# Optimization experiments

Measured on AMD Instinct MI355X. Metric: run time of the kernel, lower is better.

## Reference

```python
import jax, jax.numpy as jnp
import numpy as np

N_NODES = 100000
N_EDGES = 1600000
N_GRAPHS = 1024


def gcn_conv(x, W, b, src, dst, n_nodes):
    """PyG-style GCNConv: add self-loops, symmetric deg^-1/2 normalization,
    linear transform, scatter-add aggregation, bias."""
    h = x @ W  # [N, out]
    ones = jnp.ones(src.shape[0], dtype=h.dtype)
    deg = jax.ops.segment_sum(ones, dst, num_segments=n_nodes) + 1.0  # +1 self-loop
    dinv = jax.lax.rsqrt(deg)  # deg^-1/2, deg >= 1 so safe
    norm = dinv[src] * dinv[dst]  # [E]
    msg = h[src] * norm[:, None]  # gather + scale
    agg = jax.ops.segment_sum(msg, dst, num_segments=n_nodes)  # scatter-add
    # self-loop contribution: norm_ii = dinv_i^2
    return agg + h * (dinv * dinv)[:, None] + b


def setup_inputs() -> dict:
    key = jax.random.key(0)
    ks = jax.random.split(key, 12)
    x = jax.random.normal(ks[0], (N_NODES, 5), dtype=jnp.float32)
    src = jax.random.randint(ks[1], (N_EDGES,), 0, N_NODES)
    dst = jax.random.randint(ks[2], (N_EDGES,), 0, N_NODES)
    batch = jnp.sort(jax.random.randint(ks[3], (N_NODES,), 0, N_GRAPHS))
    def glorot(k, shp):
        lim = float(np.sqrt(6.0 / (shp[0] + shp[1])))
        return jax.random.uniform(k, shp, jnp.float32, -lim, lim)
    return {
        "x": x, "src": src, "dst": dst, "batch": batch,
        "W1": glorot(ks[4], (5, 16)),  "b1": jnp.zeros((16,), jnp.float32),
        "W2": glorot(ks[5], (16, 32)), "b2": jnp.zeros((32,), jnp.float32),
        "W3": glorot(ks[6], (32, 64)), "b3": jnp.zeros((64,), jnp.float32),
        "Wfc": glorot(ks[7], (64, 2)), "bfc": jnp.zeros((2,), jnp.float32),
    }


def reference(x, src, dst, batch, W1, b1, W2, b2, W3, b3, Wfc, bfc):
    h = jax.nn.relu(gcn_conv(x, W1, b1, src, dst, N_NODES))
    h = jax.nn.relu(gcn_conv(h, W2, b2, src, dst, N_NODES))
    h = jax.nn.relu(gcn_conv(h, W3, b3, src, dst, N_NODES))
    # global mean pool over graphs
    summed = jax.ops.segment_sum(h, batch, num_segments=N_GRAPHS)  # [G, 64]
    counts = jax.ops.segment_sum(jnp.ones(h.shape[0], h.dtype), batch, num_segments=N_GRAPHS)
    pooled = summed / jnp.maximum(counts, 1.0)[:, None]
    logits = pooled @ Wfc + bfc  # [G, 2]
    return jax.nn.log_softmax(logits, axis=1)
```

## Files before the change

### kernel.cpp

```cpp
#include <hip/hip_runtime.h>


#define BLK 256
#define CH 4096
#define EPT (CH / BLK)
#define NB 256
#define GSH 9
#define GSZ 512


__device__ inline float bfu_lo(unsigned int w) { return __uint_as_float(w << 16); }
__device__ inline float bfu_hi(unsigned int w) { return __uint_as_float(w & 0xffff0000u); }
__device__ inline unsigned int f2bf(float f) {
    unsigned int w = __float_as_uint(f);
    return (w + 0x7fffu + ((w >> 16) & 1u)) >> 16;
}
__device__ inline unsigned int pack2(float a, float b) {
    return f2bf(a) | (f2bf(b) << 16);
}


__global__ void hist1_kernel(const int* __restrict__ dst, int* __restrict__ cnt,
                             int E, int nChunks) {
    __shared__ int h[NB];
    int t = threadIdx.x, b = blockIdx.x;
    h[t] = 0;
    __syncthreads();
    int base = b * CH;
#pragma unroll
    for (int j = 0; j < EPT; ++j) {
        int e = base + j * BLK + t;
        if (e < E) atomicAdd(&h[dst[e] >> GSH], 1);
    }
    __syncthreads();
    cnt[(size_t)t * nChunks + b] = h[t];
}

__global__ void seg_scan_kernel(int* __restrict__ cnt, int* __restrict__ bucketTot,
                                int nChunks) {
    __shared__ int part[256];
    int b = blockIdx.x, t = threadIdx.x;
    size_t base = (size_t)b * nChunks;
    int per = (nChunks + 255) / 256;
    int lo = t * per, hi = lo + per < nChunks ? lo + per : nChunks;
    int sum = 0;
    for (int i = lo; i < hi; ++i) sum += cnt[base + i];
    part[t] = sum;
    __syncthreads();
    for (int off = 1; off < 256; off <<= 1) {
        int x = (t >= off) ? part[t - off] : 0;
        __syncthreads();
        if (t >= off) part[t] += x;
        __syncthreads();
    }
    int run = part[t] - sum;
    for (int i = lo; i < hi; ++i) { int v = cnt[base + i]; cnt[base + i] = run; run += v; }
    if (t == 255) bucketTot[b] = part[255];
}

__global__ void bucket_scan_kernel(const int* __restrict__ bucketTot,
                                   int* __restrict__ groupBeg, int E) {
    __shared__ int part[256];
    int t = threadIdx.x;
    int v = bucketTot[t];
    part[t] = v;
    __syncthreads();
    for (int off = 1; off < 256; off <<= 1) {
        int x = (t >= off) ? part[t - off] : 0;
        __syncthreads();
        if (t >= off) part[t] += x;
        __syncthreads();
    }
    groupBeg[t] = part[t] - v;
    if (t == 0) groupBeg[NB] = E;
}

__global__ void scatter1_kernel(const int* __restrict__ src, const int* __restrict__ dst,
                                const int* __restrict__ cnt, const int* __restrict__ groupBeg,
                                int* __restrict__ pe, int E, int nChunks) {
    __shared__ int offs[NB];
    int t = threadIdx.x, b = blockIdx.x;
    offs[t] = cnt[(size_t)t * nChunks + b] + groupBeg[t];
    __syncthreads();
    int base = b * CH;
#pragma unroll
    for (int j = 0; j < EPT; ++j) {
        int e = base + j * BLK + t;
        if (e < E) {
            int d = dst[e];
            int p = atomicAdd(&offs[d >> GSH], 1);
            pe[p] = ((d & (GSZ - 1)) << 17) | src[e];
        }
    }
}


__global__ void group_csr_kernel(const int* __restrict__ pe, const int* __restrict__ groupBeg,
                                 int* __restrict__ col, int* __restrict__ row_ptr,
                                 float* __restrict__ dinv, const float* __restrict__ x,
                                 uint4* __restrict__ xa, int N, int E) {
    __shared__ int hist[GSZ];
    __shared__ int scn[GSZ];
    __shared__ int part[256];
    int g = blockIdx.x, t = threadIdx.x;
    hist[t] = 0; hist[t + 256] = 0;
    __syncthreads();
    int lo = groupBeg[g], hi = groupBeg[g + 1];
    for (int e = lo + t; e < hi; e += BLK)
        atomicAdd(&hist[pe[e] >> 17], 1);
    __syncthreads();
    int a0 = hist[2 * t], a1 = hist[2 * t + 1];
    int s2 = a0 + a1;
    part[t] = s2;
    __syncthreads();
    for (int off = 1; off < 256; off <<= 1) {
        int xx = (t >= off) ? part[t - off] : 0;
        __syncthreads();
        if (t >= off) part[t] += xx;
        __syncthreads();
    }
    int excl = part[t] - s2;
    scn[2 * t] = excl;
    scn[2 * t + 1] = excl + a0;
    __syncthreads();
#pragma unroll
    for (int i = t; i < GSZ; i += BLK) {
        int d = (g << GSH) + i;
        if (d < N) {
            row_ptr[d] = lo + scn[i];
            float di = rsqrtf((float)hist[i] + 1.0f);
            dinv[d] = di;
            const float* r = x + (size_t)d * 5;
            uint4 u;
            u.x = pack2(r[0] * di, r[1] * di);
            u.y = pack2(r[2] * di, r[3] * di);
            u.z = pack2(r[4] * di, 0.f);
            u.w = 0u;
            xa[d] = u;
        }
    }
    if (g == 0 && t == 0) row_ptr[N] = E;
    __syncthreads();
    hist[t] = scn[t]; hist[t + 256] = scn[t + 256];
    __syncthreads();
    for (int e = lo + t; e < hi; e += BLK) {
        int v = pe[e];
        int p = atomicAdd(&hist[v >> 17], 1);
        col[lo + p] = v & 0x1FFFF;
    }
}


template <int F, int FIN, int FOUT, int CAP, bool PRESCALE_OUT>
__global__ void fused_layer_kernel(const int* __restrict__ row_ptr, const int* __restrict__ col,
                                   const uint4* __restrict__ xb, const float* __restrict__ W,
                                   const float* __restrict__ bias, const float* __restrict__ dinv,
                                   uint2* __restrict__ outb, int N) {
    constexpr int TPN = F / 8;
    constexpr int NPB = 256 / TPN;
    constexpr int RQ  = F / 8;
    constexpr int QO  = FOUT / 4;
    constexpr int STR = F + 1;
    __shared__ int lcol[CAP];
    __shared__ int lrp[NPB + 1];
    __shared__ __align__(16) float gl[NPB * STR];
    __shared__ __align__(16) float wl[FIN * FOUT];
    __shared__ __align__(16) float bl[FOUT];
    int t = threadIdx.x;
    int n0 = blockIdx.x * NPB;
    for (int i = t; i <= NPB; i += 256) lrp[i] = row_ptr[min(n0 + i, N)];
    for (int i = t; i < FIN * FOUT / 4; i += 256)
        ((float4*)wl)[i] = ((const float4*)W)[i];
    for (int i = t; i < FOUT; i += 256) bl[i] = bias[i];
    __syncthreads();
    int base = lrp[0];
    int total = lrp[NPB] - base;
    int stage = total < CAP ? total : CAP;
    for (int i = t; i < stage; i += 256) lcol[i] = col[base + i];
    __syncthreads();
    {
        int ln = t / TPN, q = t % TPN;
        int n = n0 + ln;
        if (n < N) {
            float acc[8];
            uint4 u = xb[(size_t)n * RQ + q];
            acc[0] = bfu_lo(u.x); acc[1] = bfu_hi(u.x);
            acc[2] = bfu_lo(u.y); acc[3] = bfu_hi(u.y);
            acc[4] = bfu_lo(u.z); acc[5] = bfu_hi(u.z);
            acc[6] = bfu_lo(u.w); acc[7] = bfu_hi(u.w);
            int beg = lrp[ln] - base, end = lrp[ln + 1] - base;
            int stop = end < stage ? end : stage;
            int e = beg;
            for (; e + 3 < stop; e += 4) {
                int s0 = lcol[e], s1 = lcol[e + 1], s2 = lcol[e + 2], s3 = lcol[e + 3];
                uint4 u0 = xb[(size_t)s0 * RQ + q];
                uint4 u1 = xb[(size_t)s1 * RQ + q];
                uint4 u2 = xb[(size_t)s2 * RQ + q];
                uint4 u3 = xb[(size_t)s3 * RQ + q];
                acc[0] += bfu_lo(u0.x) + bfu_lo(u1.x) + bfu_lo(u2.x) + bfu_lo(u3.x);
                acc[1] += bfu_hi(u0.x) + bfu_hi(u1.x) + bfu_hi(u2.x) + bfu_hi(u3.x);
                acc[2] += bfu_lo(u0.y) + bfu_lo(u1.y) + bfu_lo(u2.y) + bfu_lo(u3.y);
                acc[3] += bfu_hi(u0.y) + bfu_hi(u1.y) + bfu_hi(u2.y) + bfu_hi(u3.y);
                acc[4] += bfu_lo(u0.z) + bfu_lo(u1.z) + bfu_lo(u2.z) + bfu_lo(u3.z);
                acc[5] += bfu_hi(u0.z) + bfu_hi(u1.z) + bfu_hi(u2.z) + bfu_hi(u3.z);
                acc[6] += bfu_lo(u0.w) + bfu_lo(u1.w) + bfu_lo(u2.w) + bfu_lo(u3.w);
                acc[7] += bfu_hi(u0.w) + bfu_hi(u1.w) + bfu_hi(u2.w) + bfu_hi(u3.w);
            }
            for (; e < end; ++e) {
                int s = (e < stage) ? lcol[e] : col[base + e];
                uint4 uu = xb[(size_t)s * RQ + q];
                acc[0] += bfu_lo(uu.x); acc[1] += bfu_hi(uu.x);
                acc[2] += bfu_lo(uu.y); acc[3] += bfu_hi(uu.y);
                acc[4] += bfu_lo(uu.z); acc[5] += bfu_hi(uu.z);
                acc[6] += bfu_lo(uu.w); acc[7] += bfu_hi(uu.w);
            }
            float* gr = gl + ln * STR + q * 8;
#pragma unroll
            for (int j = 0; j < 8; ++j) gr[j] = acc[j];
        }
    }
    __syncthreads();
    for (int task = t; task < NPB * QO; task += 256) {
        int ln2 = task / QO, qq = task % QO;
        int n2 = n0 + ln2;
        if (n2 >= N) continue;
        float di = dinv[n2];
        const float* row = gl + ln2 * STR;
        float4 acc = make_float4(0.f, 0.f, 0.f, 0.f);
#pragma unroll
        for (int k = 0; k < FIN; ++k) {
            float rk = row[k];
            float4 wk = *(const float4*)(wl + k * FOUT + 4 * qq);
            acc.x = fmaf(rk, wk.x, acc.x);
            acc.y = fmaf(rk, wk.y, acc.y);
            acc.z = fmaf(rk, wk.z, acc.z);
            acc.w = fmaf(rk, wk.w, acc.w);
        }
        float4 bq = *(const float4*)(bl + 4 * qq);
        float4 v;
        v.x = fmaxf(di * acc.x + bq.x, 0.f);
        v.y = fmaxf(di * acc.y + bq.y, 0.f);
        v.z = fmaxf(di * acc.z + bq.z, 0.f);
        v.w = fmaxf(di * acc.w + bq.w, 0.f);
        if (PRESCALE_OUT) { v.x *= di; v.y *= di; v.z *= di; v.w *= di; }
        uint2 o;
        o.x = pack2(v.x, v.y);
        o.y = pack2(v.z, v.w);
        outb[(size_t)n2 * QO + qq] = o;
    }
}


__global__ void bounds_kernel(const int* __restrict__ batch, int* __restrict__ start,
                              int N, int G) {
    int g = blockIdx.x * blockDim.x + threadIdx.x;
    if (g > G) return;
    if (g == G) { start[G] = N; return; }
    int lo = 0, hi = N;
    while (lo < hi) {
        int mid = (lo + hi) >> 1;
        if (batch[mid] < g) lo = mid + 1; else hi = mid;
    }
    start[g] = lo;
}

__global__ void pool_head_kernel(const unsigned int* __restrict__ h, const int* __restrict__ start,
                                 const float* __restrict__ Wfc, const float* __restrict__ bfc,
                                 float* __restrict__ out) {
    __shared__ float part[8][64];
    int g = blockIdx.x;
    int t = threadIdx.x;
    int u = t & 31, w = t >> 5;
    int s = start[g], e = start[g + 1];
    float a0 = 0.f, a1 = 0.f;
    for (int n = s + w; n < e; n += 8) {
        unsigned int word = h[(size_t)n * 32 + u];
        a0 += bfu_lo(word);
        a1 += bfu_hi(word);
    }
    part[w][2 * u]     = a0;
    part[w][2 * u + 1] = a1;
    __syncthreads();
    if (t < 64) {
        float p = 0.f;
#pragma unroll
        for (int w2 = 0; w2 < 8; ++w2) p += part[w2][t];
        p /= fmaxf((float)(e - s), 1.0f);
        float l0 = p * Wfc[t * 2 + 0];
        float l1 = p * Wfc[t * 2 + 1];
#pragma unroll
        for (int off = 32; off; off >>= 1) {
            l0 += __shfl_down(l0, off);
            l1 += __shfl_down(l1, off);
        }
        if (t == 0) {
            l0 += bfc[0]; l1 += bfc[1];
            float m   = fmaxf(l0, l1);
            float lse = m + logf(expf(l0 - m) + expf(l1 - m));
            out[g * 2 + 0] = l0 - lse;
            out[g * 2 + 1] = l1 - lse;
        }
    }
}


extern "C" void kernel_launch(void* const* d_in, const int* in_sizes, int n_in,
                              void* d_out, int out_size, void* d_ws, size_t ws_size,
                              hipStream_t stream) {
    const float* x     = (const float*)d_in[0];
    const int*   src   = (const int*)d_in[1];
    const int*   dst   = (const int*)d_in[2];
    const int*   batch = (const int*)d_in[3];
    const float* W1    = (const float*)d_in[4];
    const float* b1    = (const float*)d_in[5];
    const float* W2    = (const float*)d_in[6];
    const float* b2    = (const float*)d_in[7];
    const float* W3    = (const float*)d_in[8];
    const float* b3    = (const float*)d_in[9];
    const float* Wfc   = (const float*)d_in[10];
    const float* bfc   = (const float*)d_in[11];
    float* out = (float*)d_out;

    const int N = in_sizes[0] / 5;
    const int E = in_sizes[1];
    const int G = out_size / 2;

    const int nChunks = (E + CH - 1) / CH;
    const int M       = NB * nChunks;
    const int Mpad    = (M + 3) & ~3;
    const int nGroups = (N + GSZ - 1) / GSZ;

    int* row_ptr  = (int*)d_ws;
    int* col      = row_ptr + N + 4;
    int* cnt      = col + E;
    int* groupBeg = cnt + Mpad;
    int* bucketTot= groupBeg + 260;
    int* start    = bucketTot + 256;
    float* dinv   = (float*)(start + G + 8);
    int*   Xa     = (int*)(dinv + N);
    int*   Xb     = Xa + (size_t)N * 16;
    int*   H3b    = Xb + (size_t)N * 8;
    int*   pe     = H3b;

    auto blocks = [](long n) { return (int)((n + BLK - 1) / BLK); };

    hist1_kernel<<<nChunks, 256, 0, stream>>>(dst, cnt, E, nChunks);
    seg_scan_kernel<<<NB, 256, 0, stream>>>(cnt, bucketTot, nChunks);
    bucket_scan_kernel<<<1, 256, 0, stream>>>(bucketTot, groupBeg, E);
    scatter1_kernel<<<nChunks, 256, 0, stream>>>(src, dst, cnt, groupBeg, pe, E, nChunks);
    group_csr_kernel<<<nGroups, 256, 0, stream>>>(pe, groupBeg, col, row_ptr, dinv,
                                                  x, (uint4*)Xa, N, E);

    bounds_kernel<<<blocks(G + 1), BLK, 0, stream>>>(batch, start, N, G);

    fused_layer_kernel<8, 5, 16, 6144, true><<<(N + 255) / 256, 256, 0, stream>>>(
        row_ptr, col, (const uint4*)Xa, W1, b1, dinv, (uint2*)Xb, N);

    fused_layer_kernel<16, 16, 32, 4096, true><<<(N + 127) / 128, 256, 0, stream>>>(
        row_ptr, col, (const uint4*)Xb, W2, b2, dinv, (uint2*)Xa, N);

    fused_layer_kernel<32, 32, 64, 2048, false><<<(N + 63) / 64, 256, 0, stream>>>(
        row_ptr, col, (const uint4*)Xa, W3, b3, dinv, (uint2*)H3b, N);

    pool_head_kernel<<<G, 256, 0, stream>>>((const unsigned int*)H3b, start, Wfc, bfc, out);
}
```

Measured before the change: 130.7 us.

## Replace multi-pass bucket sort with single-pass atomic bucket scatter with overflow

Collapses the histogram, two scans and scatter passes of the CSR build into one kernel. Each block claims space in fixed-capacity per-bucket slabs with a global atomic and writes into them directly, sending entries past capacity to an overflow list that the group kernel scans. The group kernel now computes bucket offsets itself by scanning the per-bucket counters. Separately, the layer kernel caches dinv in shared memory and unrolls the gather loop to 8 loads in flight. This trades launch count and memory passes for global atomic contention and nondeterministic edge order within a bucket.

```diff
diff --git a/kernel.cpp b/kernel.cpp
--- a/kernel.cpp
+++ b/kernel.cpp
@@ -7,6 +7,7 @@
 #define NB 256
 #define GSH 9
 #define GSZ 512
+#define CMAX 8192
 
 
 __device__ inline float bfu_lo(unsigned int w) { return __uint_as_float(w << 16); }
@@ -20,103 +21,81 @@
 }
 
 
-__global__ void hist1_kernel(const int* __restrict__ dst, int* __restrict__ cnt,
-                             int E, int nChunks) {
+__global__ void scatter_direct(const int* __restrict__ src, const int* __restrict__ dst,
+                               int* __restrict__ cur, int* __restrict__ pe,
+                               int2* __restrict__ ov, int* __restrict__ ovcnt, int E) {
     __shared__ int h[NB];
+    __shared__ int base[NB];
     int t = threadIdx.x, b = blockIdx.x;
     h[t] = 0;
     __syncthreads();
-    int base = b * CH;
+    int cbase = b * CH;
+    int d[EPT], s[EPT], r[EPT];
 #pragma unroll
     for (int j = 0; j < EPT; ++j) {
-        int e = base + j * BLK + t;
-        if (e < E) atomicAdd(&h[dst[e] >> GSH], 1);
-    }
-    __syncthreads();
-    cnt[(size_t)t * nChunks + b] = h[t];
-}
-
-__global__ void seg_scan_kernel(int* __restrict__ cnt, int* __restrict__ bucketTot,
-                                int nChunks) {
-    __shared__ int part[256];
-    int b = blockIdx.x, t = threadIdx.x;
-    size_t base = (size_t)b * nChunks;
-    int per = (nChunks + 255) / 256;
-    int lo = t * per, hi = lo + per < nChunks ? lo + per : nChunks;
-    int sum = 0;
-    for (int i = lo; i < hi; ++i) sum += cnt[base + i];
-    part[t] = sum;
-    __syncthreads();
-    for (int off = 1; off < 256; off <<= 1) {
-        int x = (t >= off) ? part[t - off] : 0;
-        __syncthreads();
-        if (t >= off) part[t] += x;
-        __syncthreads();
-    }
-    int run = part[t] - sum;
-    for (int i = lo; i < hi; ++i) { int v = cnt[base + i]; cnt[base + i] = run; run += v; }
-    if (t == 255) bucketTot[b] = part[255];
-}
-
-__global__ void bucket_scan_kernel(const int* __restrict__ bucketTot,
-                                   int* __restrict__ groupBeg, int E) {
-    __shared__ int part[256];
-    int t = threadIdx.x;
-    int v = bucketTot[t];
-    part[t] = v;
-    __syncthreads();
-    for (int off = 1; off < 256; off <<= 1) {
-        int x = (t >= off) ? part[t - off] : 0;
-        __syncthreads();
-        if (t >= off) part[t] += x;
-        __syncthreads();
-    }
-    groupBeg[t] = part[t] - v;
-    if (t == 0) groupBeg[NB] = E;
-}
-
-__global__ void scatter1_kernel(const int* __restrict__ src, const int* __restrict__ dst,
-                                const int* __restrict__ cnt, const int* __restrict__ groupBeg,
-                                int* __restrict__ pe, int E, int nChunks) {
-    __shared__ int offs[NB];
-    int t = threadIdx.x, b = blockIdx.x;
-    offs[t] = cnt[(size_t)t * nChunks + b] + groupBeg[t];
-    __syncthreads();
-    int base = b * CH;
+        int e = cbase + j * BLK + t;
+        bool ok = e < E;
+        d[j] = ok ? dst[e] : 0;
+        s[j] = ok ? src[e] : 0;
+        r[j] = ok ? atomicAdd(&h[d[j] >> GSH], 1) : -1;
+    }
+    __syncthreads();
+    base[t] = h[t] ? atomicAdd(&cur[t], h[t]) : 0;
+    __syncthreads();
 #pragma unroll
     for (int j = 0; j < EPT; ++j) {
-        int e = base + j * BLK + t;
-        if (e < E) {
-            int d = dst[e];
-            int p = atomicAdd(&offs[d >> GSH], 1);
-            pe[p] = ((d & (GSZ - 1)) << 17) | src[e];
-        }
-    }
-}
-
-
-__global__ void group_csr_kernel(const int* __restrict__ pe, const int* __restrict__ groupBeg,
+        if (r[j] >= 0) {
+            int bk = d[j] >> GSH;
+            int p = base[bk] + r[j];
+            if (p < CMAX) pe[bk * CMAX + p] = ((d[j] & (GSZ - 1)) << 17) | s[j];
+            else { int op = atomicAdd(ovcnt, 1); ov[op] = make_int2(d[j], s[j]); }
+        }
+    }
+}
+
+
+__global__ void group_csr_kernel(const int* __restrict__ pe, const int* __restrict__ cur,
+                                 const int2* __restrict__ ov, const int* __restrict__ ovcnt,
                                  int* __restrict__ col, int* __restrict__ row_ptr,
                                  float* __restrict__ dinv, const float* __restrict__ x,
-                                 uint4* __restrict__ xa, int N, int E) {
+                                 uint4* __restrict__ xa, int N) {
     __shared__ int hist[GSZ];
     __shared__ int scn[GSZ];
     __shared__ int part[256];
+    __shared__ int sh_gb, sh_cnt, sh_tot;
     int g = blockIdx.x, t = threadIdx.x;
+    int c = cur[t];
+    part[t] = c;
+    __syncthreads();
+    for (int off = 1; off < 256; off <<= 1) {
+        int v = (t >= off) ? part[t - off] : 0;
+        __syncthreads();
+        if (t >= off) part[t] += v;
+        __syncthreads();
+    }
+    if (t == g)   { sh_gb = part[t] - c; sh_cnt = c; }
+    if (t == 255) sh_tot = part[255];
+    __syncthreads();
+    int gb = sh_gb, mycnt = sh_cnt;
+    int nslot = mycnt < CMAX ? mycnt : CMAX;
+    int nov = *ovcnt;
     hist[t] = 0; hist[t + 256] = 0;
     __syncthreads();
-    int lo = groupBeg[g], hi = groupBeg[g + 1];
-    for (int e = lo + t; e < hi; e += BLK)
-        atomicAdd(&hist[pe[e] >> 17], 1);
+    const int* myPe = pe + g * CMAX;
+    for (int e = t; e < nslot; e += BLK) atomicAdd(&hist[myPe[e] >> 17], 1);
+    for (int i = t; i < nov; i += BLK) {
+        int2 v = ov[i];
+        if ((v.x >> GSH) == g) atomicAdd(&hist[v.x & (GSZ - 1)], 1);
+    }
     __syncthreads();
     int a0 = hist[2 * t], a1 = hist[2 * t + 1];
     int s2 = a0 + a1;
     part[t] = s2;
     __syncthreads();
     for (int off = 1; off < 256; off <<= 1) {
-        int xx = (t >= off) ? part[t - off] : 0;
+        int v = (t >= off) ? part[t - off] : 0;
         __syncthreads();
-        if (t >= off) part[t] += xx;
+        if (t >= off) part[t] += v;
         __syncthreads();
     }
     int excl = part[t] - s2;
@@ -127,7 +106,7 @@
     for (int i = t; i < GSZ; i += BLK) {
         int d = (g << GSH) + i;
         if (d < N) {
-            row_ptr[d] = lo + scn[i];
+            row_ptr[d] = gb + scn[i];
             float di = rsqrtf((float)hist[i] + 1.0f);
             dinv[d] = di;
             const float* r = x + (size_t)d * 5;
@@ -139,14 +118,21 @@
             xa[d] = u;
         }
     }
-    if (g == 0 && t == 0) row_ptr[N] = E;
+    if (g == 0 && t == 0) row_ptr[N] = sh_tot;
     __syncthreads();
     hist[t] = scn[t]; hist[t + 256] = scn[t + 256];
     __syncthreads();
-    for (int e = lo + t; e < hi; e += BLK) {
-        int v = pe[e];
+    for (int e = t; e < nslot; e += BLK) {
+        int v = myPe[e];
         int p = atomicAdd(&hist[v >> 17], 1);
-        col[lo + p] = v & 0x1FFFF;
+        col[gb + p] = v & 0x1FFFF;
+    }
+    for (int i = t; i < nov; i += BLK) {
+        int2 v = ov[i];
+        if ((v.x >> GSH) == g) {
+            int p = atomicAdd(&hist[v.x & (GSZ - 1)], 1);
+            col[gb + p] = v.y;
+        }
     }
 }
 
@@ -163,12 +149,14 @@
     constexpr int STR = F + 1;
     __shared__ int lcol[CAP];
     __shared__ int lrp[NPB + 1];
+    __shared__ float dl[NPB];
     __shared__ __align__(16) float gl[NPB * STR];
     __shared__ __align__(16) float wl[FIN * FOUT];
     __shared__ __align__(16) float bl[FOUT];
     int t = threadIdx.x;
     int n0 = blockIdx.x * NPB;
     for (int i = t; i <= NPB; i += 256) lrp[i] = row_ptr[min(n0 + i, N)];
+    for (int i = t; i < NPB; i += 256) dl[i] = dinv[min(n0 + i, N - 1)];
     for (int i = t; i < FIN * FOUT / 4; i += 256)
         ((float4*)wl)[i] = ((const float4*)W)[i];
     for (int i = t; i < FOUT; i += 256) bl[i] = bias[i];
@@ -191,20 +179,29 @@
             int beg = lrp[ln] - base, end = lrp[ln + 1] - base;
             int stop = end < stage ? end : stage;
             int e = beg;
+            for (; e + 7 < stop; e += 8) {
+                uint4 uu[8];
+#pragma unroll
+                for (int j = 0; j < 8; ++j) uu[j] = xb[(size_t)lcol[e + j] * RQ + q];
+#pragma unroll
+                for (int j = 0; j < 8; ++j) {
+                    acc[0] += bfu_lo(uu[j].x); acc[1] += bfu_hi(uu[j].x);
+                    acc[2] += bfu_lo(uu[j].y); acc[3] += bfu_hi(uu[j].y);
+                    acc[4] += bfu_lo(uu[j].z); acc[5] += bfu_hi(uu[j].z);
+                    acc[6] += bfu_lo(uu[j].w); acc[7] += bfu_hi(uu[j].w);
+                }
+            }
             for (; e + 3 < stop; e += 4) {
-                int s0 = lcol[e], s1 = lcol[e + 1], s2 = lcol[e + 2], s3 = lcol[e + 3];
-                uint4 u0 = xb[(size_t)s0 * RQ + q];
-                uint4 u1 = xb[(size_t)s1 * RQ + q];
-                uint4 u2 = xb[(size_t)s2 * RQ + q];
-                uint4 u3 = xb[(size_t)s3 * RQ + q];
-                acc[0] += bfu_lo(u0.x) + bfu_lo(u1.x) + bfu_lo(u2.x) + bfu_lo(u3.x);
-                acc[1] += bfu_hi(u0.x) + bfu_hi(u1.x) + bfu_hi(u2.x) + bfu_hi(u3.x);
-                acc[2] += bfu_lo(u0.y) + bfu_lo(u1.y) + bfu_lo(u2.y) + bfu_lo(u3.y);
-                acc[3] += bfu_hi(u0.y) + bfu_hi(u1.y) + bfu_hi(u2.y) + bfu_hi(u3.y);
-                acc[4] += bfu_lo(u0.z) + bfu_lo(u1.z) + bfu_lo(u2.z) + bfu_lo(u3.z);
-                acc[5] += bfu_hi(u0.z) + bfu_hi(u1.z) + bfu_hi(u2.z) + bfu_hi(u3.z);
-                acc[6] += bfu_lo(u0.w) + bfu_lo(u1.w) + bfu_lo(u2.w) + bfu_lo(u3.w);
-                acc[7] += bfu_hi(u0.w) + bfu_hi(u1.w) + bfu_hi(u2.w) + bfu_hi(u3.w);
+                uint4 uu[4];
+#pragma unroll
+                for (int j = 0; j < 4; ++j) uu[j] = xb[(size_t)lcol[e + j] * RQ + q];
+#pragma unroll
+                for (int j = 0; j < 4; ++j) {
+                    acc[0] += bfu_lo(uu[j].x); acc[1] += bfu_hi(uu[j].x);
+                    acc[2] += bfu_lo(uu[j].y); acc[3] += bfu_hi(uu[j].y);
+                    acc[4] += bfu_lo(uu[j].z); acc[5] += bfu_hi(uu[j].z);
+                    acc[6] += bfu_lo(uu[j].w); acc[7] += bfu_hi(uu[j].w);
+                }
             }
             for (; e < end; ++e) {
                 int s = (e < stage) ? lcol[e] : col[base + e];
@@ -224,7 +221,7 @@
         int ln2 = task / QO, qq = task % QO;
         int n2 = n0 + ln2;
         if (n2 >= N) continue;
-        float di = dinv[n2];
+        float di = dl[ln2];
         const float* row = gl + ln2 * STR;
         float4 acc = make_float4(0.f, 0.f, 0.f, 0.f);
 #pragma unroll
@@ -326,32 +323,27 @@
     const int G = out_size / 2;
 
     const int nChunks = (E + CH - 1) / CH;
-    const int M       = NB * nChunks;
-    const int Mpad    = (M + 3) & ~3;
-    const int nGroups = (N + GSZ - 1) / GSZ;
+    const int nGroups = (N + GSZ - 1) >> GSH;
 
     int* row_ptr  = (int*)d_ws;
     int* col      = row_ptr + N + 4;
-    int* cnt      = col + E;
-    int* groupBeg = cnt + Mpad;
-    int* bucketTot= groupBeg + 260;
-    int* start    = bucketTot + 256;
+    int* cur      = col + E;
+    int* ovcnt    = cur + 256;
+    int* start    = cur + 260;
     float* dinv   = (float*)(start + G + 8);
     int*   Xa     = (int*)(dinv + N);
     int*   Xb     = Xa + (size_t)N * 16;
     int*   H3b    = Xb + (size_t)N * 8;
-    int*   pe     = H3b;
+    int*   pe     = H3b + (size_t)N * 32;
+    int2*  ov     = (int2*)H3b;
 
     auto blocks = [](long n) { return (int)((n + BLK - 1) / BLK); };
 
-    hist1_kernel<<<nChunks, 256, 0, stream>>>(dst, cnt, E, nChunks);
-    seg_scan_kernel<<<NB, 256, 0, stream>>>(cnt, bucketTot, nChunks);
-    bucket_scan_kernel<<<1, 256, 0, stream>>>(bucketTot, groupBeg, E);
-    scatter1_kernel<<<nChunks, 256, 0, stream>>>(src, dst, cnt, groupBeg, pe, E, nChunks);
-    group_csr_kernel<<<nGroups, 256, 0, stream>>>(pe, groupBeg, col, row_ptr, dinv,
-                                                  x, (uint4*)Xa, N, E);
-
+    hipMemsetAsync(cur, 0, 260 * sizeof(int), stream);
+    scatter_direct<<<nChunks, 256, 0, stream>>>(src, dst, cur, pe, ov, ovcnt, E);
     bounds_kernel<<<blocks(G + 1), BLK, 0, stream>>>(batch, start, N, G);
+    group_csr_kernel<<<nGroups, 256, 0, stream>>>(pe, cur, ov, ovcnt, col, row_ptr,
+                                                  dinv, x, (uint4*)Xa, N);
 
     fused_layer_kernel<8, 5, 16, 6144, true><<<(N + 255) / 256, 256, 0, stream>>>(
         row_ptr, col, (const uint4*)Xa, W1, b1, dinv, (uint2*)Xb, N);
```

Measured after the change: 154.7 us. 1.18x slower.
